# Performance work log

Hardware: AMD Instinct MI355X
Metric: run time of the kernel (lower is better)

Reference implementation:

```python
import jax, jax.numpy as jnp
import numpy as np

N = 50000   # query points
M = 50000   # support points
H = 32      # neighbors per query
K = 15      # kernel points
C = 128     # channels (in == out)
P = 3       # spatial dim
RADIUS = 2.5
KP_EXTENT = 1.2


def setup_inputs() -> dict:
    key = jax.random.key(0)
    ks = jax.random.split(key, 6)
    q_pts = jax.random.normal(ks[0], (N, P), dtype=jnp.float32)
    s_pts = jax.random.normal(ks[1], (M, P), dtype=jnp.float32)
    neighb_inds = jax.random.randint(ks[2], (N, H), 0, M, dtype=jnp.int64)
    x = jax.random.normal(ks[3], (N, C), dtype=jnp.float32)
    # kernel points fixed inside the sphere of given radius
    kernel_points = jax.random.uniform(ks[4], (K, P), dtype=jnp.float32,
                                       minval=-RADIUS, maxval=RADIUS) * 0.5
    # dw_weights init: normal(std=sqrt(1/K)) as in reset_parameters
    dw_weights = jax.random.normal(ks[5], (K, C), dtype=jnp.float32) * np.sqrt(1.0 / K)
    bias = jnp.zeros((C,), dtype=jnp.float32)
    return {"q_pts": q_pts, "s_pts": s_pts, "neighb_inds": neighb_inds,
            "x": x, "kernel_points": kernel_points,
            "dw_weights": dw_weights, "bias": bias}


def reference(q_pts, s_pts, neighb_inds, x, kernel_points, dw_weights, bias):
    # pad support points with a far-away point (index M) and features with zeros
    s_pad = jnp.concatenate([s_pts, jnp.full((1, s_pts.shape[1]), 1e6, s_pts.dtype)], axis=0)
    x_pad = jnp.concatenate([x, jnp.zeros((1, x.shape[1]), x.dtype)], axis=0)

    neighbors = s_pad[neighb_inds] - q_pts[:, None, :]            # [N,H,P]
    diff = neighbors[:, :, None, :] - kernel_points               # [N,H,K,P]
    sq_d = jnp.sum(diff * diff, axis=-1)                          # [N,H,K]
    all_w = jax.nn.relu(1.0 - jnp.sqrt(sq_d) / KP_EXTENT)         # linear KP influence

    neighb_x = x_pad[neighb_inds]                                 # [N,H,C]
    # matmul(all_weights^T, neighb_x): [N,K,H] @ [N,H,C] -> [N,K,C]
    weighted = jnp.einsum('nhk,nhc->nkc', all_w, neighb_x)
    # depthwise multiply by dw_weights [K,C] then sum over kernel points
    result = jnp.einsum('nkc,kc->nc', weighted, dw_weights) + bias
    return result
```

## Files before the change

### kernel.cpp

```cpp
#include <hip/hip_runtime.h>
#include <hip/hip_bf16.h>

#define N_Q 50000
#define H_NB 32
#define K_KP 15
#define C_CH 128
#define KP_EXT 1.2f

typedef __attribute__((ext_vector_type(8))) short bf16x8;
typedef __attribute__((ext_vector_type(4))) float f32x4;

static __device__ __forceinline__ short f2bf(float f) {
    __hip_bfloat16 h = __float2bfloat16(f);
    return *reinterpret_cast<short*>(&h);
}

__global__ __launch_bounds__(256)
void cvt_perm_kernel(const float* __restrict__ x, const float* __restrict__ s_pts,
                     ushort* __restrict__ xb, float4* __restrict__ sp4) {
    const int t  = threadIdx.x;
    const int m  = blockIdx.x * 16 + (t >> 4);
    const int ln = t & 15;
    const float* xr = x + (size_t)m * C_CH;
    uint v[8];
#pragma unroll
    for (int i = 0; i < 8; ++i)
        v[i] = (uint)(ushort)f2bf(xr[ln + 16 * i]);
    uint4 o;
    o.x = v[0] | (v[1] << 16);
    o.y = v[2] | (v[3] << 16);
    o.z = v[4] | (v[5] << 16);
    o.w = v[6] | (v[7] << 16);
    *(uint4*)(xb + (size_t)m * C_CH + ln * 8) = o;
    if (ln == 0) {
        sp4[m] = make_float4(s_pts[3*m], s_pts[3*m+1], s_pts[3*m+2], 0.f);
    }
}

__global__ __launch_bounds__(256, 8)
void kpconv_mfma4(const float* __restrict__ q_pts,
                  const float4* __restrict__ sp4,
                  const int*   __restrict__ inds,
                  const ushort* __restrict__ xb,
                  const float* __restrict__ kp,
                  const float* __restrict__ dw,
                  const float* __restrict__ bias,
                  float*       __restrict__ out)
{
    const int wave = threadIdx.x >> 6;
    const int l    = threadIdx.x & 63;
    const int n    = blockIdx.x * 4 + wave;
    const int lg   = l >> 4;
    const int ln   = l & 15;

    const int4* ip = (const int4*)(inds + n * H_NB + lg * 8);
    const int4 i0 = ip[0], i1 = ip[1];
    const int idxv[8] = {i0.x,i0.y,i0.z,i0.w,i1.x,i1.y,i1.z,i1.w};

    uint4 rv[8];
#pragma unroll
    for (int j = 0; j < 8; ++j)
        rv[j] = *(const uint4*)(xb + (size_t)(unsigned)idxv[j] * C_CH + ln * 8);

    const float qx = q_pts[n*3+0], qy = q_pts[n*3+1], qz = q_pts[n*3+2];
    const int kkc = ln < K_KP ? ln : (K_KP - 1);
    const float ox = qx + kp[kkc*3+0];
    const float oy = qy + kp[kkc*3+1];
    const float oz = qz + kp[kkc*3+2];

    bf16x8 afrag;
#pragma unroll
    for (int j = 0; j < 8; ++j) {
        const float4 p = sp4[(unsigned)idxv[j]];
        const float dx = p.x - ox, dy = p.y - oy, dz = p.z - oz;
        const float d  = sqrtf(fmaf(dx, dx, fmaf(dy, dy, dz*dz)));
        float w = fmaxf(1.0f - d * (1.0f/KP_EXT), 0.0f);
        if (ln == 15) w = 0.0f;
        afrag[j] = f2bf(w);
    }

    f32x4 acc[8];
#pragma unroll
    for (int t = 0; t < 8; ++t) acc[t] = (f32x4){0.f, 0.f, 0.f, 0.f};

    const uint* rw = (const uint*)&rv[0];
#pragma unroll
    for (int t = 0; t < 8; ++t) {
        const uint sel = (t & 1) ? 0x07060302u : 0x05040100u;
        const int  w   = t >> 1;
        union { bf16x8 v; uint u[4]; } bf;
#pragma unroll
        for (int r = 0; r < 4; ++r) {
            bf.u[r] = __builtin_amdgcn_perm(rw[(2*r+1)*4 + w], rw[(2*r)*4 + w], sel);
        }
        acc[t] = __builtin_amdgcn_mfma_f32_16x16x32_bf16(afrag, bf.v, acc[t], 0, 0, 0);
    }

    const int rowbase = lg * 4;
#pragma unroll
    for (int t = 0; t < 8; ++t) {
        const int c = t*16 + ln;
        float s = 0.f;
#pragma unroll
        for (int r = 0; r < 4; ++r) {
            const int row = rowbase + r;
            const float dwv = (row < K_KP) ? dw[row * C_CH + c] : 0.f;
            s = fmaf(dwv, acc[t][r], s);
        }
        s += __shfl_xor(s, 16);
        s += __shfl_xor(s, 32);
        s += bias[c];
        if (l < 16) out[n * C_CH + c] = s;
    }
}

__global__ __launch_bounds__(256, 4)
void kpconv_mfma_fb(const float* __restrict__ q_pts,
                    const float* __restrict__ s_pts,
                    const int*   __restrict__ inds,
                    const float* __restrict__ x,
                    const float* __restrict__ kp,
                    const float* __restrict__ dw,
                    const float* __restrict__ bias,
                    float*       __restrict__ out)
{
    const int wave = threadIdx.x >> 6;
    const int l    = threadIdx.x & 63;
    const int n    = blockIdx.x * 4 + wave;
    const int lg   = l >> 4;
    const int ln   = l & 15;

    const int4* ip = (const int4*)(inds + n * H_NB + lg * 8);
    const int4 i0 = ip[0], i1 = ip[1];
    const int idxv[8] = {i0.x,i0.y,i0.z,i0.w,i1.x,i1.y,i1.z,i1.w};

    const float qx = q_pts[n*3+0], qy = q_pts[n*3+1], qz = q_pts[n*3+2];
    const int kkc = ln < K_KP ? ln : (K_KP - 1);
    const float kpx = kp[kkc*3+0], kpy = kp[kkc*3+1], kpz = kp[kkc*3+2];

    bf16x8 afrag;
#pragma unroll
    for (int j = 0; j < 8; ++j) {
        const int idx = idxv[j];
        const float px = s_pts[idx*3+0] - qx;
        const float py = s_pts[idx*3+1] - qy;
        const float pz = s_pts[idx*3+2] - qz;
        const float dx = px - kpx, dy = py - kpy, dz = pz - kpz;
        const float d  = sqrtf(fmaf(dx, dx, fmaf(dy, dy, dz*dz)));
        float w = fmaxf(1.0f - d * (1.0f/KP_EXT), 0.0f);
        if (ln == 15) w = 0.0f;
        afrag[j] = f2bf(w);
    }

    unsigned boff[8];
#pragma unroll
    for (int j = 0; j < 8; ++j) boff[j] = (unsigned)idxv[j] * C_CH + (unsigned)ln;

    f32x4 acc[8];
#pragma unroll
    for (int t = 0; t < 8; ++t) acc[t] = (f32x4){0.f, 0.f, 0.f, 0.f};
#pragma unroll
    for (int t = 0; t < 8; ++t) {
        bf16x8 bfrag;
#pragma unroll
        for (int j = 0; j < 8; ++j) bfrag[j] = f2bf(x[boff[j] + t*16]);
        acc[t] = __builtin_amdgcn_mfma_f32_16x16x32_bf16(afrag, bfrag, acc[t], 0, 0, 0);
    }

    const int rowbase = lg * 4;
#pragma unroll
    for (int t = 0; t < 8; ++t) {
        const int c = t*16 + ln;
        float s = 0.f;
#pragma unroll
        for (int r = 0; r < 4; ++r) {
            const int row = rowbase + r;
            const float dwv = (row < K_KP) ? dw[row * C_CH + c] : 0.f;
            s = fmaf(dwv, acc[t][r], s);
        }
        s += __shfl_xor(s, 16);
        s += __shfl_xor(s, 32);
        s += bias[c];
        if (l < 16) out[n * C_CH + c] = s;
    }
}

extern "C" void kernel_launch(void* const* d_in, const int* in_sizes, int n_in,
                              void* d_out, int out_size, void* d_ws, size_t ws_size,
                              hipStream_t stream) {
    const float* q_pts = (const float*)d_in[0];
    const float* s_pts = (const float*)d_in[1];
    const int*   inds  = (const int*)  d_in[2];
    const float* x     = (const float*)d_in[3];
    const float* kp    = (const float*)d_in[4];
    const float* dw    = (const float*)d_in[5];
    const float* bias  = (const float*)d_in[6];
    float* out = (float*)d_out;

    const size_t xb_bytes  = (size_t)N_Q * C_CH * sizeof(ushort);
    const size_t sp4_bytes = (size_t)N_Q * sizeof(float4);

    if (ws_size >= xb_bytes + sp4_bytes) {
        ushort* xb  = (ushort*)d_ws;
        float4* sp4 = (float4*)((char*)d_ws + xb_bytes);
        cvt_perm_kernel<<<N_Q / 16, 256, 0, stream>>>(x, s_pts, xb, sp4);
        kpconv_mfma4<<<N_Q / 4, 256, 0, stream>>>(q_pts, sp4, inds, xb,
                                                  kp, dw, bias, out);
    } else {
        kpconv_mfma_fb<<<N_Q / 4, 256, 0, stream>>>(q_pts, s_pts, inds, x,
                                                    kp, dw, bias, out);
    }
}
```

Baseline: 173.8 us.

## Split each query across two waves and prepack q, kernel points, dw weights

The main kernel now gives each query point two waves, each handling half the channels (64), which halves per-wave register use and gather width and doubles the wave count. The prep kernel also packs q_pts into float4, precomputes clamped kernel points, and lays out dw weights in per-lane float4 order, so the epilogue needs one vector load instead of four predicated scalar loads. In exchange, the neighbor-index loads and kernel-weight computation run twice per query, and the gathers become 8-byte accesses instead of 16-byte ones.

After: 170.3 us. 2.0% less time.

```diff
diff --git a/kernel.cpp b/kernel.cpp
--- a/kernel.cpp
+++ b/kernel.cpp
@@ -16,8 +16,12 @@
 }
 
 __global__ __launch_bounds__(256)
-void cvt_perm_kernel(const float* __restrict__ x, const float* __restrict__ s_pts,
-                     ushort* __restrict__ xb, float4* __restrict__ sp4) {
+void prep_kernel(const float* __restrict__ x, const float* __restrict__ s_pts,
+                 const float* __restrict__ q_pts, const float* __restrict__ kp,
+                 const float* __restrict__ dw,
+                 ushort* __restrict__ xb, float4* __restrict__ sp4,
+                 float4* __restrict__ q4, float4* __restrict__ kp4,
+                 float4* __restrict__ dwp2) {
     const int t  = threadIdx.x;
     const int m  = blockIdx.x * 16 + (t >> 4);
     const int ln = t & 15;
@@ -32,24 +36,43 @@
     o.z = v[4] | (v[5] << 16);
     o.w = v[6] | (v[7] << 16);
     *(uint4*)(xb + (size_t)m * C_CH + ln * 8) = o;
-    if (ln == 0) {
+    if (ln == 0)
         sp4[m] = make_float4(s_pts[3*m], s_pts[3*m+1], s_pts[3*m+2], 0.f);
+    if (ln == 1)
+        q4[m] = make_float4(q_pts[3*m], q_pts[3*m+1], q_pts[3*m+2], 0.f);
+    if (blockIdx.x == 0) {
+        if (t < 16) {
+            const int kk = t < K_KP ? t : (K_KP - 1);
+            kp4[t] = make_float4(kp[3*kk], kp[3*kk+1], kp[3*kk+2], 0.f);
+        }
+        for (int s = t; s < 512; s += 256) {
+            const int lane = s & 63, half = (s >> 6) & 1, t4 = s >> 7;
+            const int lgg = lane >> 4, lnn = lane & 15;
+            const int c = half * 64 + t4 * 16 + lnn;
+            float4 w;
+            w.x = dw[(lgg*4 + 0) * C_CH + c];
+            w.y = dw[(lgg*4 + 1) * C_CH + c];
+            w.z = dw[(lgg*4 + 2) * C_CH + c];
+            w.w = (lgg*4 + 3 < K_KP) ? dw[(lgg*4 + 3) * C_CH + c] : 0.f;
+            dwp2[s] = w;
+        }
     }
 }
 
 __global__ __launch_bounds__(256, 8)
-void kpconv_mfma4(const float* __restrict__ q_pts,
+void kpconv_mfma5(const float4* __restrict__ q4,
                   const float4* __restrict__ sp4,
-                  const int*   __restrict__ inds,
+                  const int*    __restrict__ inds,
                   const ushort* __restrict__ xb,
-                  const float* __restrict__ kp,
-                  const float* __restrict__ dw,
-                  const float* __restrict__ bias,
-                  float*       __restrict__ out)
+                  const float4* __restrict__ kp4,
+                  const float4* __restrict__ dwp2,
+                  const float*  __restrict__ bias,
+                  float*        __restrict__ out)
 {
     const int wave = threadIdx.x >> 6;
     const int l    = threadIdx.x & 63;
-    const int n    = blockIdx.x * 4 + wave;
+    const int n    = blockIdx.x * 2 + (wave >> 1);
+    const int half = wave & 1;
     const int lg   = l >> 4;
     const int ln   = l & 15;
 
@@ -57,16 +80,14 @@
     const int4 i0 = ip[0], i1 = ip[1];
     const int idxv[8] = {i0.x,i0.y,i0.z,i0.w,i1.x,i1.y,i1.z,i1.w};
 
-    uint4 rv[8];
+    uint2 rv[8];
 #pragma unroll
     for (int j = 0; j < 8; ++j)
-        rv[j] = *(const uint4*)(xb + (size_t)(unsigned)idxv[j] * C_CH + ln * 8);
-
-    const float qx = q_pts[n*3+0], qy = q_pts[n*3+1], qz = q_pts[n*3+2];
-    const int kkc = ln < K_KP ? ln : (K_KP - 1);
-    const float ox = qx + kp[kkc*3+0];
-    const float oy = qy + kp[kkc*3+1];
-    const float oz = qz + kp[kkc*3+2];
+        rv[j] = *(const uint2*)(xb + (size_t)(unsigned)idxv[j] * C_CH + ln * 8 + half * 4);
+
+    const float4 qn = q4[n];
+    const float4 k4 = kp4[ln];
+    const float ox = qn.x + k4.x, oy = qn.y + k4.y, oz = qn.z + k4.z;
 
     bf16x8 afrag;
 #pragma unroll
@@ -79,38 +100,35 @@
         afrag[j] = f2bf(w);
     }
 
-    f32x4 acc[8];
-#pragma unroll
-    for (int t = 0; t < 8; ++t) acc[t] = (f32x4){0.f, 0.f, 0.f, 0.f};
+    f32x4 acc[4];
+#pragma unroll
+    for (int t = 0; t < 4; ++t) acc[t] = (f32x4){0.f, 0.f, 0.f, 0.f};
 
     const uint* rw = (const uint*)&rv[0];
 #pragma unroll
-    for (int t = 0; t < 8; ++t) {
+    for (int t = 0; t < 4; ++t) {
         const uint sel = (t & 1) ? 0x07060302u : 0x05040100u;
         const int  w   = t >> 1;
         union { bf16x8 v; uint u[4]; } bf;
 #pragma unroll
-        for (int r = 0; r < 4; ++r) {
-            bf.u[r] = __builtin_amdgcn_perm(rw[(2*r+1)*4 + w], rw[(2*r)*4 + w], sel);
-        }
+        for (int r = 0; r < 4; ++r)
+            bf.u[r] = __builtin_amdgcn_perm(rw[(2*r+1)*2 + w], rw[(2*r)*2 + w], sel);
         acc[t] = __builtin_amdgcn_mfma_f32_16x16x32_bf16(afrag, bf.v, acc[t], 0, 0, 0);
     }
 
-    const int rowbase = lg * 4;
-#pragma unroll
-    for (int t = 0; t < 8; ++t) {
-        const int c = t*16 + ln;
-        float s = 0.f;
-#pragma unroll
-        for (int r = 0; r < 4; ++r) {
-            const int row = rowbase + r;
-            const float dwv = (row < K_KP) ? dw[row * C_CH + c] : 0.f;
-            s = fmaf(dwv, acc[t][r], s);
-        }
+    const int cbase = half * 64;
+#pragma unroll
+    for (int t = 0; t < 4; ++t) {
+        const float4 dwd = dwp2[(t*2 + half) * 64 + l];
+        float s;
+        s = dwd.x * acc[t][0];
+        s = fmaf(dwd.y, acc[t][1], s);
+        s = fmaf(dwd.z, acc[t][2], s);
+        s = fmaf(dwd.w, acc[t][3], s);
         s += __shfl_xor(s, 16);
         s += __shfl_xor(s, 32);
-        s += bias[c];
-        if (l < 16) out[n * C_CH + c] = s;
+        s += bias[cbase + t*16 + ln];
+        if (l < 16) out[n * C_CH + cbase + t*16 + ln] = s;
     }
 }
 
@@ -197,15 +215,23 @@
     const float* bias  = (const float*)d_in[6];
     float* out = (float*)d_out;
 
-    const size_t xb_bytes  = (size_t)N_Q * C_CH * sizeof(ushort);
-    const size_t sp4_bytes = (size_t)N_Q * sizeof(float4);
-
-    if (ws_size >= xb_bytes + sp4_bytes) {
-        ushort* xb  = (ushort*)d_ws;
-        float4* sp4 = (float4*)((char*)d_ws + xb_bytes);
-        cvt_perm_kernel<<<N_Q / 16, 256, 0, stream>>>(x, s_pts, xb, sp4);
-        kpconv_mfma4<<<N_Q / 4, 256, 0, stream>>>(q_pts, sp4, inds, xb,
-                                                  kp, dw, bias, out);
+    const size_t xb_b   = (size_t)N_Q * C_CH * sizeof(ushort);
+    const size_t sp4_b  = (size_t)N_Q * sizeof(float4);
+    const size_t q4_b   = (size_t)N_Q * sizeof(float4);
+    const size_t kp4_b  = 16 * sizeof(float4);
+    const size_t dwp2_b = 512 * sizeof(float4);
+
+    if (ws_size >= xb_b + sp4_b + q4_b + kp4_b + dwp2_b) {
+        char* p = (char*)d_ws;
+        ushort* xb   = (ushort*)p;                 p += xb_b;
+        float4* sp4  = (float4*)p;                 p += sp4_b;
+        float4* q4   = (float4*)p;                 p += q4_b;
+        float4* kp4  = (float4*)p;                 p += kp4_b;
+        float4* dwp2 = (float4*)p;
+        prep_kernel<<<N_Q / 16, 256, 0, stream>>>(x, s_pts, q_pts, kp, dw,
+                                                  xb, sp4, q4, kp4, dwp2);
+        kpconv_mfma5<<<N_Q / 2, 256, 0, stream>>>(q4, sp4, inds, xb,
+                                                  kp4, dwp2, bias, out);
     } else {
         kpconv_mfma_fb<<<N_Q / 4, 256, 0, stream>>>(q_pts, s_pts, inds, x,
                                                     kp, dw, bias, out);
```
